# Optimization experiments

Hardware: AMD Instinct MI355X
Metric: run time of the kernel (lower is better)

## Reference

```python
import jax, jax.numpy as jnp
import numpy as np

B, H0, W0, DIM, DS = 8, 64, 64, 256, 16
HID = int(DIM * 2.0)          # d_inner of the scan (expand=1 on hidden)
DTR = -(-HID // 16)           # dt_rank = ceil(hidden/16) = 32
SCALE = 1.0                   # block residual scale
EPS = 1e-5


def _ln(x, g, b):
    m = x.mean(-1, keepdims=True)
    v = ((x - m) ** 2).mean(-1, keepdims=True)
    return (x - m) * jax.lax.rsqrt(v + EPS) * g + b


def _conv(x, k, groups=1):  # NCHW, OIHW, padding=1 (SAME for 3x3)
    return jax.lax.conv_general_dilated(x, k, (1, 1), 'SAME', feature_group_count=groups)


def _selective_scan(u, delta, A, Bs, Cs, D):
    # u, delta: [B,Dh,L]; A: [Dh,Ns]; Bs, Cs: [B,Ns,L]; D: [Dh]
    uT = jnp.moveaxis(u, 2, 0)      # [L,B,Dh]
    dT = jnp.moveaxis(delta, 2, 0)  # [L,B,Dh]
    bT = jnp.moveaxis(Bs, 2, 0)     # [L,B,Ns]
    cT = jnp.moveaxis(Cs, 2, 0)     # [L,B,Ns]
    h0 = jnp.zeros((u.shape[0], u.shape[1], A.shape[1]), u.dtype)

    def step(h, inp):
        u_t, d_t, b_t, c_t = inp
        h = jnp.exp(d_t[:, :, None] * A) * h + (d_t * u_t)[:, :, None] * b_t[:, None, :]
        return h, jnp.einsum('bdn,bn->bd', h, c_t)

    _, ys = jax.lax.scan(step, h0, (uT, dT, bT, cT))
    return jnp.moveaxis(ys, 0, 1) + jnp.moveaxis(u, 1, 2) * D  # [B,L,Dh]


def setup_inputs() -> dict:
    key = jax.random.key(0)
    ks = jax.random.split(key, 24)
    r = lambda i, s, sc=0.02: jax.random.normal(ks[i], s, jnp.float32) * sc
    dt = jnp.exp(jax.random.uniform(ks[20], (HID,)) * (np.log(0.1) - np.log(0.001)) + np.log(0.001))
    dt_b = dt + jnp.log(-jnp.expm1(-dt))  # inverse-softplus init of dt bias
    A_logs = jnp.log(jnp.tile(jnp.arange(1, DS + 1, dtype=jnp.float32), (HID, 1)))  # [HID,DS]
    return {
        'x': jax.random.normal(ks[0], (B, H0 * W0, DIM), jnp.float32),
        'norm1_g': jnp.ones(DIM), 'norm1_b': jnp.zeros(DIM),
        'fusion_w': r(1, (3,), 0.3),
        'prio_scale': jnp.float32(1.0), 'prio_offset': jnp.float32(0.0),
        'in_w': r(2, (HID, DIM)), 'in_b': jnp.zeros(HID),
        'cpe_w': r(3, (HID, 1, 3, 3), 0.1), 'cpe_b': jnp.zeros(HID),
        'x_proj_w': r(4, (DTR + 2 * DS, HID)),
        'dt_w': r(5, (HID, DTR), DTR ** -0.5), 'dt_b': dt_b,
        'A_logs': A_logs, 'Ds': jnp.ones(HID),
        'gC_w': r(6, (DS,), 0.1), 'gC_b': jnp.zeros(DS),
        'gC_weight': jnp.float32(0.1),
        'outn_g': jnp.ones(HID), 'outn_b': jnp.zeros(HID),
        'outp_w': r(7, (DIM, HID)), 'outp_b': jnp.zeros(DIM),
        'norm2_g': jnp.ones(DIM), 'norm2_b': jnp.zeros(DIM),
        'mlp_w1': r(8, (HID, DIM)), 'mlp_b1': jnp.zeros(HID),
        'mlp_w2': r(9, (DIM, HID)), 'mlp_b2': jnp.zeros(DIM),
        'H': H0, 'W': W0,
    }


def reference(x, norm1_g, norm1_b, fusion_w, prio_scale, prio_offset, in_w, in_b,
              cpe_w, cpe_b, x_proj_w, dt_w, dt_b, A_logs, Ds, gC_w, gC_b, gC_weight,
              outn_g, outn_b, outp_w, outp_b, norm2_g, norm2_b,
              mlp_w1, mlp_b1, mlp_w2, mlp_b2, H, W):
    Bsz, N, C = x.shape
    # ---- gradient extractor ----
    xs = jnp.transpose(x, (0, 2, 1)).reshape(Bsz, C, H, W)
    gray = xs.mean(1, keepdims=True)
    sob_x = jnp.array([[-1, 0, 1], [-2, 0, 2], [-1, 0, 1]], jnp.float32)[None, None]
    sob_y = jnp.array([[-1, -2, -1], [0, 0, 0], [1, 2, 1]], jnp.float32)[None, None]
    lap = jnp.array([[0, -1, 0], [-1, 4, -1], [0, -1, 0]], jnp.float32)[None, None]
    grads = jnp.concatenate([_conv(gray, sob_x), _conv(gray, sob_y), _conv(gray, lap)], 1)
    gm = jnp.abs(jnp.einsum('c,bchw->bhw', fusion_w, grads))  # 1x1 fusion, no bias
    # ---- gradient -> priority ----
    gf = gm.reshape(Bsz, -1)
    gmin = gf.min(1, keepdims=True); gmax = gf.max(1, keepdims=True)
    gp = jax.nn.sigmoid(prio_scale * ((gf - gmin) / (gmax - gmin + 1e-8)) + prio_offset)  # [B,N]
    # ---- gradient-guided mamba branch ----
    idx = jnp.argsort(gp, axis=-1)       # sort tokens by priority
    inv = jnp.argsort(idx, axis=-1)      # inverse permutation
    xn = _ln(x, norm1_g, norm1_b)
    xp = jnp.einsum('bnc,hc->bnh', xn, in_w) + in_b              # 1x1 in_proj -> [B,N,HID]
    xp_sp = jnp.transpose(xp, (0, 2, 1)).reshape(Bsz, HID, H, W)
    cpe = _conv(xp_sp, cpe_w, groups=HID) + cpe_b[None, :, None, None]
    gated = xp_sp * jax.nn.sigmoid(cpe)
    tok = jnp.transpose(gated.reshape(Bsz, HID, N), (0, 2, 1))   # [B,N,HID]
    sx = jnp.take_along_axis(tok, idx[:, :, None], axis=1)       # semantic_neighbor
    # ---- SSM core ----
    u = jnp.transpose(sx, (0, 2, 1))                             # [B,HID,L]
    x_dbl = jnp.einsum('bdl,cd->bcl', u, x_proj_w)
    dts, Bm, Cm = jnp.split(x_dbl, [DTR, DTR + DS], axis=1)
    delta = jax.nn.softplus(jnp.einsum('brl,dr->bdl', dts, dt_w) + dt_b[None, :, None])
    ge = gp[:, :, None] * gC_w + gC_b                            # Linear(1,DS): [B,L,DS]
    Cm = Cm + gC_weight * ge.reshape(Bsz, DS, N)                 # faithful to torch .view(B,K,DS,L)
    A = -jnp.exp(A_logs)
    y = _selective_scan(u, delta, A, Bm, Cm, Ds)                 # [B,L,HID]
    y = _ln(y, outn_g, outn_b) @ outp_w.T + outp_b               # [B,L,DIM]
    x_out = jnp.take_along_axis(y, inv[:, :, None], axis=1)     # un-sort
    x1 = x + SCALE * x_out
    # ---- MLP branch ----
    h = _ln(x1, norm2_g, norm2_b)
    h = jax.nn.silu(h @ mlp_w1.T + mlp_b1) @ mlp_w2.T + mlp_b2
    return x1 + SCALE * h
```

## Files before the change

### kernel.cpp

```cpp
#include <hip/hip_runtime.h>
#include <hip/hip_bf16.h>

typedef __hip_bfloat16 bf16;

static constexpr int BSZ  = 8;
static constexpr int L    = 4096;
static constexpr int DIMC = 256;
static constexpr int HID  = 512;
static constexpr int NCH  = 64;
static constexpr int CLEN = 64;
static constexpr int MROWS = BSZ * L;

typedef __attribute__((ext_vector_type(8))) short bf16x8;
typedef __attribute__((ext_vector_type(4))) short short4v;
typedef __attribute__((ext_vector_type(4))) float f32x4;

__device__ __forceinline__ short f2b(float f) {
    return __builtin_bit_cast(short, __float2bfloat16(f));
}
__device__ __forceinline__ float b2f(bf16 v) { return __bfloat162float(v); }
__device__ __forceinline__ float s2f(short s) {
    return __bfloat162float(__builtin_bit_cast(bf16, s));
}
__device__ __forceinline__ float fexp2(float x) {
    float r;
    asm("v_exp_f32 %0, %1" : "=v"(r) : "v"(x));
    return r;
}
__device__ __forceinline__ void gload_lds16(const void* g, void* l) {
    __builtin_amdgcn_global_load_lds(
        (const __attribute__((address_space(1))) unsigned int*)g,
        (__attribute__((address_space(3))) unsigned int*)l, 16, 0, 0);
}

__global__ void gray_kernel(const float* __restrict__ x, float* __restrict__ gray) {
    int gid = blockIdx.x * blockDim.x + threadIdx.x;
    int wid = gid >> 6, lane = gid & 63;
    if (wid >= MROWS) return;
    float4 f = *(const float4*)(x + (size_t)wid * DIMC + lane * 4);
    float s = f.x + f.y + f.z + f.w;
    for (int o = 32; o; o >>= 1) s += __shfl_down(s, o);
    if (lane == 0) gray[wid] = s * (1.f / 256.f);
}

__global__ void grad_kernel(const float* __restrict__ gray, float* __restrict__ gm,
                            const float* __restrict__ fw) {
    int p = blockIdx.x * blockDim.x + threadIdx.x;
    if (p >= MROWS) return;
    int b = p >> 12, pp = p & 4095, h = pp >> 6, w = pp & 63;
    const float* g = gray + ((size_t)b << 12);
    auto G = [&](int hh, int ww) -> float {
        if (hh < 0 || hh > 63 || ww < 0 || ww > 63) return 0.f;
        return g[(hh << 6) + ww];
    };
    float g00=G(h-1,w-1), g01=G(h-1,w), g02=G(h-1,w+1);
    float g10=G(h,  w-1), g11=G(h,  w), g12=G(h,  w+1);
    float g20=G(h+1,w-1), g21=G(h+1,w), g22=G(h+1,w+1);
    float gx  = -g00 + g02 - 2.f*g10 + 2.f*g12 - g20 + g22;
    float gy  = -g00 - 2.f*g01 - g02 + g20 + 2.f*g21 + g22;
    float lap = 4.f*g11 - g01 - g10 - g12 - g21;
    float v = fw[0]*gx + fw[1]*gy + fw[2]*lap;
    gm[p] = fabsf(v);
}

__global__ __launch_bounds__(1024) void gp_kernel(float* __restrict__ gmgp,
                                                  const float* __restrict__ sc_,
                                                  const float* __restrict__ of_) {
    int b = blockIdx.x, tid = threadIdx.x;
    float v[4], lmin = 3.4e38f, lmax = -3.4e38f;
    for (int i = 0; i < 4; i++) {
        v[i] = gmgp[(b << 12) + tid + (i << 10)];
        lmin = fminf(lmin, v[i]); lmax = fmaxf(lmax, v[i]);
    }
    for (int o = 32; o; o >>= 1) {
        lmin = fminf(lmin, __shfl_xor(lmin, o));
        lmax = fmaxf(lmax, __shfl_xor(lmax, o));
    }
    __shared__ float smin[16], smax[16];
    int wid = tid >> 6, lane = tid & 63;
    if (lane == 0) { smin[wid] = lmin; smax[wid] = lmax; }
    __syncthreads();
    if (tid == 0) {
        float a = smin[0], c = smax[0];
        for (int wv = 1; wv < 16; wv++) { a = fminf(a, smin[wv]); c = fmaxf(c, smax[wv]); }
        smin[0] = a; smax[0] = c;
    }
    __syncthreads();
    float gmin = smin[0], gmax = smax[0];
    float invd = 1.f / (gmax - gmin + 1e-8f);
    float sc = sc_[0], of = of_[0];
    for (int i = 0; i < 4; i++) {
        float z = sc * ((v[i] - gmin) * invd) + of;
        gmgp[(b << 12) + tid + (i << 10)] = 1.f / (1.f + __expf(-z));
    }
}

__global__ __launch_bounds__(1024) void sort_kernel(const float* __restrict__ gp,
                                                    int* __restrict__ idx, int* __restrict__ inv) {
    __shared__ unsigned long long keys[4096];
    int b = blockIdx.x, tid = threadIdx.x;
    for (int i = tid; i < 4096; i += 1024) {
        unsigned int fb = __float_as_uint(gp[(b << 12) + i]);
        keys[i] = ((unsigned long long)fb << 32) | (unsigned int)i;
    }
    __syncthreads();
    for (int k = 2; k <= 4096; k <<= 1) {
        for (int j = k >> 1; j > 0; j >>= 1) {
            for (int i = tid; i < 4096; i += 1024) {
                int ixj = i ^ j;
                if (ixj > i) {
                    unsigned long long a = keys[i], c = keys[ixj];
                    bool up = ((i & k) == 0);
                    if ((a > c) == up) { keys[i] = c; keys[ixj] = a; }
                }
            }
            __syncthreads();
        }
    }
    for (int i = tid; i < 4096; i += 1024) {
        int p = (int)(keys[i] & 0xffffffffULL);
        idx[(b << 12) + i] = p;
        inv[(b << 12) + p] = i;
    }
}

__global__ void normf_k(const float* __restrict__ src, const float* __restrict__ g,
                        const float* __restrict__ b, short* __restrict__ dst) {
    int gid = blockIdx.x * blockDim.x + threadIdx.x;
    int wid = gid >> 6, lane = gid & 63;
    if (wid >= MROWS) return;
    float4 f = *(const float4*)(src + (size_t)wid * 256 + lane * 4);
    float v[4] = {f.x, f.y, f.z, f.w};
    float s = v[0] + v[1] + v[2] + v[3];
    for (int o = 32; o; o >>= 1) s += __shfl_xor(s, o);
    float mean = s * (1.f / 256.f);
    float q = 0.f;
    for (int i = 0; i < 4; i++) { float d = v[i] - mean; q += d * d; }
    for (int o = 32; o; o >>= 1) q += __shfl_xor(q, o);
    float rstd = rsqrtf(q * (1.f / 256.f) + 1e-5f);
    short4v ov;
    for (int i = 0; i < 4; i++)
        ov[i] = f2b((v[i] - mean) * rstd * g[lane * 4 + i] + b[lane * 4 + i]);
    *(short4v*)(dst + (size_t)wid * 256 + lane * 4) = ov;
}

__global__ void normb_k(const short* __restrict__ src, const float* __restrict__ g,
                        const float* __restrict__ b, short* __restrict__ dst) {
    int gid = blockIdx.x * blockDim.x + threadIdx.x;
    int wid = gid >> 6, lane = gid & 63;
    if (wid >= MROWS) return;
    bf16x8 pk = *(const bf16x8*)(src + (size_t)wid * 512 + lane * 8);
    float v[8];
    for (int i = 0; i < 8; i++) v[i] = s2f(pk[i]);
    float s = 0.f;
    for (int i = 0; i < 8; i++) s += v[i];
    for (int o = 32; o; o >>= 1) s += __shfl_xor(s, o);
    float mean = s * (1.f / 512.f);
    float q = 0.f;
    for (int i = 0; i < 8; i++) { float d = v[i] - mean; q += d * d; }
    for (int o = 32; o; o >>= 1) q += __shfl_xor(q, o);
    float rstd = rsqrtf(q * (1.f / 512.f) + 1e-5f);
    bf16x8 ov;
    for (int i = 0; i < 8; i++)
        ov[i] = f2b((v[i] - mean) * rstd * g[lane * 8 + i] + b[lane * 8 + i]);
    *(bf16x8*)(dst + (size_t)wid * 512 + lane * 8) = ov;
}

__global__ void wbig_k(const float* __restrict__ dtw, const float* __restrict__ xpw,
                       short* __restrict__ wd) {
    int d = blockIdx.x;
    for (int kk = threadIdx.x; kk < HID; kk += 256) {
        float s = 0.f;
        if (d < 512) {
#pragma unroll
            for (int r = 0; r < 32; r++) s += dtw[d * 32 + r] * xpw[r * HID + kk];
        } else if (d < 544) {
            s = xpw[(d - 480) * HID + kk];
        }
        wd[(size_t)d * HID + kk] = f2b(s);
    }
}

__global__ void wcvt_k(const float* __restrict__ s0, const float* __restrict__ s1,
                       const float* __restrict__ s2, const float* __restrict__ s3,
                       short* __restrict__ dst) {
    int g = blockIdx.x * blockDim.x + threadIdx.x;
    if (g >= 524288) return;
    float v;
    if      (g < 131072) v = s0[g];
    else if (g < 262144) v = s1[g - 131072];
    else if (g < 393216) v = s2[g - 262144];
    else                 v = s3[g - 393216];
    dst[g] = f2b(v);
}

enum { EP_BF = 0, EP_DELTAXBC = 1, EP_SILU = 2, EP_SCATTER = 3, EP_RESID = 4 };

template<int NBX, int KT, int EP>
__global__ __launch_bounds__(256) void mgemm(
    const short* __restrict__ A, int lda, const short* __restrict__ W,
    const float* __restrict__ bias, int N,
    const int* __restrict__ idx, const float* __restrict__ xres, const float* __restrict__ fres,
    float* __restrict__ outf, bf16* __restrict__ outb)
{
    __shared__ __align__(16) short As[3][128 * 32];
    __shared__ __align__(16) short Bs[3][128 * 32];

    const int t = threadIdx.x;
    const int id = blockIdx.x;
    const int xcd = id & 7, sl = id >> 3;
    const int bx = sl % NBX, byl = sl / NBX;
    const int m0 = (xcd * 32 + byl) << 7, n0 = bx << 7;

    const int w = t >> 6, lane = t & 63;
    const int wm0 = (w & 1) << 6, wn0 = (w >> 1) << 6;
    const int lrow = lane & 15, quad = lane >> 4;
    const int wbase = t & ~63;

    int r0 = t >> 2, r1 = (256 + t) >> 2;
    int q0 = (t & 3) ^ ((r0 >> 1) & 3);
    int q1 = (t & 3) ^ ((r1 >> 1) & 3);
    const short* Asrc0 = A + (size_t)(m0 + r0) * lda + q0 * 8;
    const short* Asrc1 = A + (size_t)(m0 + r1) * lda + q1 * 8;
    const short* Wsrc0 = W + (size_t)(n0 + r0) * KT + q0 * 8;
    const short* Wsrc1 = W + (size_t)(n0 + r1) * KT + q1 * 8;

    constexpr int nK = KT / 32;
    f32x4 acc[4][4] = {};

    auto stage = [&](int k, int buf) {
        gload_lds16(Asrc0 + k * 32, &As[buf][wbase * 8]);
        gload_lds16(Asrc1 + k * 32, &As[buf][(256 + wbase) * 8]);
        gload_lds16(Wsrc0 + k * 32, &Bs[buf][wbase * 8]);
        gload_lds16(Wsrc1 + k * 32, &Bs[buf][(256 + wbase) * 8]);
    };

    stage(0, 0);
    stage(1, 1);
#pragma unroll
    for (int kk = 0; kk < nK; kk++) {
        if (kk + 1 < nK) asm volatile("s_waitcnt vmcnt(4)" ::: "memory");
        else             asm volatile("s_waitcnt vmcnt(0)" ::: "memory");
        __builtin_amdgcn_s_barrier();
        const int cur = kk % 3;
        bf16x8 af[4], bfr[4];
#pragma unroll
        for (int f = 0; f < 4; f++) {
            int r = wm0 + f * 16 + lrow;
            af[f] = *(const bf16x8*)&As[cur][r * 32 + ((quad ^ ((r >> 1) & 3)) << 3)];
        }
#pragma unroll
        for (int g = 0; g < 4; g++) {
            int r = wn0 + g * 16 + lrow;
            bfr[g] = *(const bf16x8*)&Bs[cur][r * 32 + ((quad ^ ((r >> 1) & 3)) << 3)];
        }
        if (kk + 2 < nK) stage(kk + 2, (kk + 2) % 3);
        __builtin_amdgcn_s_setprio(1);
#pragma unroll
        for (int f = 0; f < 4; f++)
#pragma unroll
            for (int g = 0; g < 4; g++)
                acc[f][g] = __builtin_amdgcn_mfma_f32_16x16x32_bf16(bfr[g], af[f], acc[f][g], 0, 0, 0);
        __builtin_amdgcn_s_setprio(0);
    }

#pragma unroll
    for (int f = 0; f < 4; f++) {
        int row = m0 + wm0 + f * 16 + lrow;
#pragma unroll
        for (int g = 0; g < 4; g++) {
            int ch = n0 + wn0 + g * 16 + quad * 4;
            f32x4 v4 = acc[f][g];
            if (EP == EP_DELTAXBC) {
                if (ch < 512) {
                    float4 b4 = *(const float4*)&bias[ch];
                    float vv[4] = {v4[0] + b4.x, v4[1] + b4.y, v4[2] + b4.z, v4[3] + b4.w};
                    short4v ov;
#pragma unroll
                    for (int i = 0; i < 4; i++) {
                        float sp = (vv[i] > 20.f) ? vv[i] : __logf(1.f + __expf(vv[i]));
                        ov[i] = f2b(sp);
                    }
                    *(short4v*)((short*)outb + (size_t)row * HID + ch) = ov;
                } else if (ch < 544) {
                    *(f32x4*)(outf + (size_t)row * 32 + (ch - 512)) = v4;
                }
            } else {
                if (bias) {
                    float4 b4 = *(const float4*)&bias[ch];
                    v4[0] += b4.x; v4[1] += b4.y; v4[2] += b4.z; v4[3] += b4.w;
                }
                if (EP == EP_SILU) {
#pragma unroll
                    for (int i = 0; i < 4; i++) v4[i] = v4[i] / (1.f + __expf(-v4[i]));
                }
                if (EP == EP_SCATTER) {
                    int bb = row >> 12;
                    int p = idx[row];
                    size_t o = (((size_t)bb << 12) + p) * (size_t)N + ch;
                    float4 xr = *(const float4*)(xres + o);
                    float4 ov = {xr.x + v4[0], xr.y + v4[1], xr.z + v4[2], xr.w + v4[3]};
                    *(float4*)(outf + o) = ov;
                } else if (EP == EP_RESID) {
                    size_t o = (size_t)row * N + ch;
                    float4 fr = *(const float4*)(fres + o);
                    float4 ov = {fr.x + v4[0], fr.y + v4[1], fr.z + v4[2], fr.w + v4[3]};
                    *(float4*)(outf + o) = ov;
                } else {
                    short4v ov;
#pragma unroll
                    for (int i = 0; i < 4; i++) ov[i] = f2b(v4[i]);
                    *(short4v*)((short*)outb + (size_t)row * N + ch) = ov;
                }
            }
        }
    }
}

__global__ __launch_bounds__(256) void cpe_kernel(const bf16* __restrict__ xp,
                                                  const float* __restrict__ cw,
                                                  const float* __restrict__ cb,
                                                  const int* __restrict__ inv,
                                                  bf16* __restrict__ sx) {
    __shared__ float4 smem[8 * 325];
    const int blk = blockIdx.x;
    const int cg = blk & 15, tile = (blk >> 4) & 15, b = blk >> 8;
    const int h0 = (tile >> 2) << 4, w0 = (tile & 3) << 4;
    const int cg0 = cg << 5;
    const int t = threadIdx.x;

    for (int i = 0; i < 11; i++) {
        int lin = i * 256 + t;
        if (lin < 2592) {
            int pix = lin >> 3, c = lin & 7;
            int hh = pix / 18, ww = pix - hh * 18;
            int gh = h0 + hh - 1, gw = w0 + ww - 1;
            float4 val = {0.f, 0.f, 0.f, 0.f};
            if (gh >= 0 && gh < 64 && gw >= 0 && gw < 64) {
                short4v s = *(const short4v*)((const short*)xp +
                    ((size_t)((b << 12) + (gh << 6) + gw)) * HID + cg0 + c * 4);
                val.x = s2f(s[0]); val.y = s2f(s[1]); val.z = s2f(s[2]); val.w = s2f(s[3]);
            }
            smem[c * 325 + pix] = val;
        }
    }
    __syncthreads();

    const int c = t & 7, pg = t >> 3;
    const int ch0 = cg0 + c * 4;
    float4 wk[9], cb4;
#pragma unroll
    for (int ki = 0; ki < 9; ki++) {
        wk[ki].x = cw[(ch0 + 0) * 9 + ki];
        wk[ki].y = cw[(ch0 + 1) * 9 + ki];
        wk[ki].z = cw[(ch0 + 2) * 9 + ki];
        wk[ki].w = cw[(ch0 + 3) * 9 + ki];
    }
    cb4.x = cb[ch0]; cb4.y = cb[ch0 + 1]; cb4.z = cb[ch0 + 2]; cb4.w = cb[ch0 + 3];

    for (int k = 0; k < 8; k++) {
        int pix = pg + k * 32;
        int h = pix >> 4, w = pix & 15;
        int hp = (h + 1) * 18 + (w + 1);
        float ax = 0.f, ay = 0.f, az = 0.f, aw = 0.f;
#pragma unroll
        for (int dh = -1; dh <= 1; dh++)
#pragma unroll
            for (int dw = -1; dw <= 1; dw++) {
                float4 v = smem[c * 325 + hp + dh * 18 + dw];
                float4 wt = wk[(dh + 1) * 3 + (dw + 1)];
                ax += v.x * wt.x; ay += v.y * wt.y; az += v.z * wt.z; aw += v.w * wt.w;
            }
        ax += cb4.x; ay += cb4.y; az += cb4.z; aw += cb4.w;
        float4 xv = smem[c * 325 + hp];
        short4v g;
        g[0] = f2b(xv.x / (1.f + __expf(-ax)));
        g[1] = f2b(xv.y / (1.f + __expf(-ay)));
        g[2] = f2b(xv.z / (1.f + __expf(-az)));
        g[3] = f2b(xv.w / (1.f + __expf(-aw)));
        int pglob = (b << 12) + ((h0 + h) << 6) + (w0 + w);
        int r = inv[pglob];
        *(short4v*)((short*)sx + ((size_t)((b << 12) + r)) * HID + ch0) = g;
    }
}

__global__ void gcfix_kernel(float* __restrict__ xdbl, const float* __restrict__ gp,
                             const float* __restrict__ gw_, const float* __restrict__ gcw,
                             const float* __restrict__ gcb) {
    int i = blockIdx.x * blockDim.x + threadIdx.x;
    int s = i & 15, t = (i >> 4) & 4095, b = i >> 16;
    float gw = gw_[0];
    float gpv = gp[(b << 12) + (s << 8) + (t >> 4)];
    int tm = t & 15;
    xdbl[(((size_t)(b << 12) + t) << 5) + 16 + s] += gw * (gpv * gcw[tm] + gcb[tm]);
}

__global__ __launch_bounds__(1024) void scan_pass1(const bf16* __restrict__ delta,
                                                   const bf16* __restrict__ sx,
                                                   const float* __restrict__ xdbl,
                                                   const float* __restrict__ A_logs,
                                                   float* __restrict__ h_end,
                                                   float* __restrict__ sumdelta) {
    __shared__ float Bsm[CLEN][16];
    int b = blockIdx.x >> 6, c = blockIdx.x & 63;
    int tid = threadIdx.x;
    int d = tid >> 1, half = tid & 1, s0 = half << 3;
    int t0 = c << 6;
    {
        int row = tid >> 4, col = tid & 15;
        Bsm[row][col] = xdbl[(((size_t)(b << 12) + t0 + row) << 5) + col];
    }
    __syncthreads();
    float A2[8];
#pragma unroll
    for (int s = 0; s < 8; s++)
        A2[s] = -__expf(A_logs[d * 16 + s0 + s]) * 1.442695040888963f;
    float h[8];
#pragma unroll
    for (int s = 0; s < 8; s++) h[s] = 0.f;
    float sumd = 0.f;
    size_t base = (((size_t)b << 12) + t0) * HID + d;
    for (int tb = 0; tb < CLEN; tb += 8) {
        float dl[8], uu[8];
#pragma unroll
        for (int j = 0; j < 8; j++) {
            size_t ro = base + (size_t)(tb + j) * HID;
            dl[j] = b2f(delta[ro]);
            uu[j] = b2f(sx[ro]);
        }
#pragma unroll
        for (int j = 0; j < 8; j++) {
            int t = tb + j;
            float dlt = dl[j];
            sumd += dlt;
            float du = dlt * uu[j];
#pragma unroll
            for (int s = 0; s < 8; s++)
                h[s] = fexp2(A2[s] * dlt) * h[s] + du * Bsm[t][s0 + s];
        }
    }
    int cidx = blockIdx.x;
    if (half == 0) sumdelta[(size_t)cidx * HID + d] = sumd;
#pragma unroll
    for (int s = 0; s < 8; s++)
        h_end[((size_t)cidx * 16 + s0 + s) * HID + d] = h[s];
}

__global__ __launch_bounds__(512) void scan_combine(float* __restrict__ hbuf,
                                                    const float* __restrict__ sumdelta,
                                                    const float* __restrict__ A_logs) {
    int b = blockIdx.x >> 4, s = blockIdx.x & 15, d = threadIdx.x;
    float A2 = -__expf(A_logs[d * 16 + s]) * 1.442695040888963f;
    float carry = 0.f;
    int cidx0 = b << 6;
    float sd_n = sumdelta[(size_t)cidx0 * HID + d];
    float he_n = hbuf[((size_t)cidx0 * 16 + s) * HID + d];
    for (int c = 0; c < NCH; c++) {
        int cidx = cidx0 + c;
        float sd = sd_n, he = he_n;
        if (c + 1 < NCH) {
            sd_n = sumdelta[(size_t)(cidx + 1) * HID + d];
            he_n = hbuf[((size_t)(cidx + 1) * 16 + s) * HID + d];
        }
        hbuf[((size_t)cidx * 16 + s) * HID + d] = carry;
        carry = fexp2(A2 * sd) * carry + he;
    }
}

__global__ __launch_bounds__(1024) void scan_pass2(const bf16* __restrict__ delta,
                                                   bf16* __restrict__ sxy,
                                                   const float* __restrict__ xdbl,
                                                   const float* __restrict__ A_logs,
                                                   const float* __restrict__ Ds,
                                                   const float* __restrict__ h_start) {
    __shared__ float BC[CLEN][32];
    int b = blockIdx.x >> 6, c = blockIdx.x & 63;
    int tid = threadIdx.x;
    int d = tid >> 1, half = tid & 1, s0 = half << 3;
    int t0 = c << 6;
#pragma unroll
    for (int i = tid; i < CLEN * 32; i += 1024) {
        int row = i >> 5, col = i & 31;
        BC[row][col] = xdbl[(((size_t)(b << 12) + t0 + row) << 5) + col];
    }
    __syncthreads();
    float A2[8];
#pragma unroll
    for (int s = 0; s < 8; s++)
        A2[s] = -__expf(A_logs[d * 16 + s0 + s]) * 1.442695040888963f;
    int cidx = blockIdx.x;
    float h[8];
#pragma unroll
    for (int s = 0; s < 8; s++)
        h[s] = h_start[((size_t)cidx * 16 + s0 + s) * HID + d];
    float Dd = Ds[d];
    size_t base = (((size_t)b << 12) + t0) * HID + d;
    for (int tb = 0; tb < CLEN; tb += 8) {
        float dl[8], uu[8];
#pragma unroll
        for (int j = 0; j < 8; j++) {
            size_t ro = base + (size_t)(tb + j) * HID;
            dl[j] = b2f(delta[ro]);
            uu[j] = b2f(sxy[ro]);
        }
#pragma unroll
        for (int j = 0; j < 8; j++) {
            int t = tb + j;
            float dlt = dl[j];
            float du = dlt * uu[j];
            float acc = half ? 0.f : uu[j] * Dd;
#pragma unroll
            for (int s = 0; s < 8; s++) {
                h[s] = fexp2(A2[s] * dlt) * h[s] + du * BC[t][s0 + s];
                acc += h[s] * BC[t][16 + s0 + s];
            }
            float other = __shfl_xor(acc, 1);
            acc += other;
            if (half == 0)
                sxy[base + (size_t)t * HID] = __float2bfloat16(acc);
        }
    }
}

extern "C" void kernel_launch(void* const* d_in, const int* in_sizes, int n_in,
                              void* d_out, int out_size, void* d_ws, size_t ws_size,
                              hipStream_t stream) {
    const float* x        = (const float*)d_in[0];
    const float* norm1_g  = (const float*)d_in[1];
    const float* norm1_b  = (const float*)d_in[2];
    const float* fusion_w = (const float*)d_in[3];
    const float* prio_sc  = (const float*)d_in[4];
    const float* prio_of  = (const float*)d_in[5];
    const float* in_w     = (const float*)d_in[6];
    const float* in_b     = (const float*)d_in[7];
    const float* cpe_w    = (const float*)d_in[8];
    const float* cpe_b    = (const float*)d_in[9];
    const float* xproj_w  = (const float*)d_in[10];
    const float* dt_w     = (const float*)d_in[11];
    const float* dt_b     = (const float*)d_in[12];
    const float* A_logs   = (const float*)d_in[13];
    const float* Ds       = (const float*)d_in[14];
    const float* gC_w     = (const float*)d_in[15];
    const float* gC_b     = (const float*)d_in[16];
    const float* gC_wt    = (const float*)d_in[17];
    const float* outn_g   = (const float*)d_in[18];
    const float* outn_b   = (const float*)d_in[19];
    const float* outp_w   = (const float*)d_in[20];
    const float* outp_b   = (const float*)d_in[21];
    const float* norm2_g  = (const float*)d_in[22];
    const float* norm2_b  = (const float*)d_in[23];
    const float* mlp_w1   = (const float*)d_in[24];
    const float* mlp_b1   = (const float*)d_in[25];
    const float* mlp_w2   = (const float*)d_in[26];
    const float* mlp_b2   = (const float*)d_in[27];
    float* out = (float*)d_out;

    float* ws = (float*)d_ws;
    size_t off = 0;
    auto alloc = [&](size_t n) { float* p = ws + off; off += (n + 63) & ~(size_t)63; return p; };
    float* gray   = alloc(MROWS);
    float* gp     = alloc(MROWS);
    int*   idxb   = (int*)alloc(MROWS);
    int*   invb   = (int*)alloc(MROWS);
    float* xdbl   = alloc((size_t)MROWS * 32);
    short* wbig   = (short*)alloc((size_t)640 * HID / 2);
    short* wbuf   = (short*)alloc(524288 / 2);
    short* xn     = (short*)alloc((size_t)MROWS * DIMC / 2);
    float* sumd   = alloc((size_t)BSZ * NCH * HID);
    float* hbuf   = alloc((size_t)BSZ * NCH * 16 * HID);
    bf16*  bufA   = (bf16*)alloc((size_t)MROWS * HID / 2);
    bf16*  bufB   = (bf16*)alloc((size_t)MROWS * HID / 2);
    float* bufC   = alloc((size_t)MROWS * DIMC);
    if (off * sizeof(float) > ws_size) return;

    short* w_in  = wbuf;
    short* w_out = wbuf + 131072;
    short* w_m1  = wbuf + 262144;
    short* w_m2  = wbuf + 393216;

    wcvt_k<<<(524288 + 255) / 256, 256, 0, stream>>>(in_w, outp_w, mlp_w1, mlp_w2, wbuf);
    wbig_k<<<640, 256, 0, stream>>>(dt_w, xproj_w, wbig);

    gray_kernel<<<MROWS / 4, 256, 0, stream>>>(x, gray);
    grad_kernel<<<MROWS / 256, 256, 0, stream>>>(gray, gp, fusion_w);
    gp_kernel<<<BSZ, 1024, 0, stream>>>(gp, prio_sc, prio_of);
    sort_kernel<<<BSZ, 1024, 0, stream>>>(gp, idxb, invb);

    normf_k<<<MROWS / 4, 256, 0, stream>>>(x, norm1_g, norm1_b, xn);
    mgemm<4, 256, EP_BF><<<4 * 256, 256, 0, stream>>>(
        xn, DIMC, w_in, in_b, HID, nullptr, nullptr, nullptr, nullptr, bufA);

    cpe_kernel<<<BSZ * 16 * 16, 256, 0, stream>>>(bufA, cpe_w, cpe_b, invb, bufB);

    mgemm<5, 512, EP_DELTAXBC><<<5 * 256, 256, 0, stream>>>(
        (const short*)bufB, HID, wbig, dt_b, 640, nullptr, nullptr, nullptr, xdbl, bufA);
    gcfix_kernel<<<(MROWS * 16) / 256, 256, 0, stream>>>(xdbl, gp, gC_wt, gC_w, gC_b);

    scan_pass1<<<BSZ * NCH, 1024, 0, stream>>>(bufA, bufB, xdbl, A_logs, hbuf, sumd);
    scan_combine<<<BSZ * 16, 512, 0, stream>>>(hbuf, sumd, A_logs);
    scan_pass2<<<BSZ * NCH, 1024, 0, stream>>>(bufA, bufB, xdbl, A_logs, Ds, hbuf);

    normb_k<<<MROWS / 4, 256, 0, stream>>>((const short*)bufB, outn_g, outn_b, (short*)bufA);
    mgemm<2, 512, EP_SCATTER><<<2 * 256, 256, 0, stream>>>(
        (const short*)bufA, HID, w_out, outp_b, DIMC, idxb, x, nullptr, bufC, nullptr);

    normf_k<<<MROWS / 4, 256, 0, stream>>>(bufC, norm2_g, norm2_b, (short*)bufB);
    mgemm<4, 256, EP_SILU><<<4 * 256, 256, 0, stream>>>(
        (const short*)bufB, DIMC, w_m1, mlp_b1, HID, nullptr, nullptr, nullptr, nullptr, bufA);
    mgemm<2, 512, EP_RESID><<<2 * 256, 256, 0, stream>>>(
        (const short*)bufA, HID, w_m2, mlp_b2, DIMC, nullptr, nullptr, bufC, out, nullptr);
}
```

Baseline: 511.1 us.

## Replace single-block bitonic sort with parallel rank-count sort across many blocks

Replaces the per-batch bitonic sort, which ran on only one block per batch with many barrier stages, by a brute-force rank computation. Tiles of keys are compared against shared-memory key tiles to produce partial counts. A second kernel sums the partial counts into ranks and scatters idx and inv. This spreads the sort across far more compute units at the cost of O(N^2) comparisons and an extra workspace buffer and launch.

Result: faster. 469.2 us (-8.2%).

```diff
diff --git a/kernel.cpp b/kernel.cpp
--- a/kernel.cpp
+++ b/kernel.cpp
@@ -95,33 +95,49 @@
     }
 }
 
-__global__ __launch_bounds__(1024) void sort_kernel(const float* __restrict__ gp,
-                                                    int* __restrict__ idx, int* __restrict__ inv) {
-    __shared__ unsigned long long keys[4096];
-    int b = blockIdx.x, tid = threadIdx.x;
-    for (int i = tid; i < 4096; i += 1024) {
-        unsigned int fb = __float_as_uint(gp[(b << 12) + i]);
-        keys[i] = ((unsigned long long)fb << 32) | (unsigned int)i;
+__global__ __launch_bounds__(256) void rank_kernel(const float* __restrict__ gp,
+                                                   unsigned int* __restrict__ part) {
+    __shared__ unsigned long long jk[512];
+    int blk = blockIdx.x, t = threadIdx.x;
+    int b = blk >> 5, it = (blk >> 3) & 3, jt = blk & 7;
+    int j0 = jt << 9;
+    {
+        float2 f2 = *(const float2*)(gp + (b << 12) + j0 + t * 2);
+        jk[t * 2]     = ((unsigned long long)__float_as_uint(f2.x) << 32) | (unsigned)(j0 + t * 2);
+        jk[t * 2 + 1] = ((unsigned long long)__float_as_uint(f2.y) << 32) | (unsigned)(j0 + t * 2 + 1);
     }
     __syncthreads();
-    for (int k = 2; k <= 4096; k <<= 1) {
-        for (int j = k >> 1; j > 0; j >>= 1) {
-            for (int i = tid; i < 4096; i += 1024) {
-                int ixj = i ^ j;
-                if (ixj > i) {
-                    unsigned long long a = keys[i], c = keys[ixj];
-                    bool up = ((i & k) == 0);
-                    if ((a > c) == up) { keys[i] = c; keys[ixj] = a; }
-                }
-            }
-            __syncthreads();
-        }
-    }
-    for (int i = tid; i < 4096; i += 1024) {
-        int p = (int)(keys[i] & 0xffffffffULL);
-        idx[(b << 12) + i] = p;
-        inv[(b << 12) + p] = i;
-    }
+    int i0 = (it << 10) + t * 4;
+    float4 f4 = *(const float4*)(gp + (b << 12) + i0);
+    unsigned long long ki[4];
+    ki[0] = ((unsigned long long)__float_as_uint(f4.x) << 32) | (unsigned)(i0 + 0);
+    ki[1] = ((unsigned long long)__float_as_uint(f4.y) << 32) | (unsigned)(i0 + 1);
+    ki[2] = ((unsigned long long)__float_as_uint(f4.z) << 32) | (unsigned)(i0 + 2);
+    ki[3] = ((unsigned long long)__float_as_uint(f4.w) << 32) | (unsigned)(i0 + 3);
+    unsigned int c0 = 0, c1 = 0, c2 = 0, c3 = 0;
+#pragma unroll 8
+    for (int j = 0; j < 512; j++) {
+        unsigned long long kj = jk[j];
+        c0 += kj < ki[0];
+        c1 += kj < ki[1];
+        c2 += kj < ki[2];
+        c3 += kj < ki[3];
+    }
+    uint4 o = {c0, c1, c2, c3};
+    *(uint4*)&part[(((size_t)b * 8 + jt) << 12) + i0] = o;
+}
+
+__global__ void rscatter_kernel(const unsigned int* __restrict__ part,
+                                int* __restrict__ idx, int* __restrict__ inv) {
+    int i = blockIdx.x * blockDim.x + threadIdx.x;
+    if (i >= MROWS) return;
+    int b = i >> 12, il = i & 4095;
+    unsigned int r = 0;
+#pragma unroll
+    for (int jt = 0; jt < 8; jt++)
+        r += part[(((size_t)b * 8 + jt) << 12) + il];
+    idx[(b << 12) + r] = il;
+    inv[(b << 12) + il] = r;
 }
 
 __global__ void normf_k(const float* __restrict__ src, const float* __restrict__ g,
@@ -562,6 +578,7 @@
     float* gp     = alloc(MROWS);
     int*   idxb   = (int*)alloc(MROWS);
     int*   invb   = (int*)alloc(MROWS);
+    unsigned int* rpart = (unsigned int*)alloc((size_t)BSZ * 8 * 4096);
     float* xdbl   = alloc((size_t)MROWS * 32);
     short* wbig   = (short*)alloc((size_t)640 * HID / 2);
     short* wbuf   = (short*)alloc(524288 / 2);
@@ -584,7 +601,8 @@
     gray_kernel<<<MROWS / 4, 256, 0, stream>>>(x, gray);
     grad_kernel<<<MROWS / 256, 256, 0, stream>>>(gray, gp, fusion_w);
     gp_kernel<<<BSZ, 1024, 0, stream>>>(gp, prio_sc, prio_of);
-    sort_kernel<<<BSZ, 1024, 0, stream>>>(gp, idxb, invb);
+    rank_kernel<<<BSZ * 4 * 8, 256, 0, stream>>>(gp, rpart);
+    rscatter_kernel<<<MROWS / 256, 256, 0, stream>>>(rpart, idxb, invb);
 
     normf_k<<<MROWS / 4, 256, 0, stream>>>(x, norm1_g, norm1_b, xn);
     mgemm<4, 256, EP_BF><<<4 * 256, 256, 0, stream>>>(
```
